# Optimization experiments

Measured on AMD Instinct MI355X. Metric: run time of the kernel, lower is better.

Reference implementation:

```python
import jax, jax.numpy as jnp
import numpy as np

B, M, N, R, FD = 128, 64, 64, 8, 128
BN_EPS = 1e-5
GS_EPS = 1e-8


def conv2d(x, w, b):
    # x: [B,C,H,W], w: [O,C,3,3] or [O,C,1,1]
    y = jax.lax.conv_general_dilated(x, w, (1, 1), 'SAME',
                                     dimension_numbers=('NCHW', 'OIHW', 'NCHW'))
    return y + b[None, :, None, None]


def complex_conv(x, wr, br, wi, bi):
    cr = conv2d(x, wr, br)
    ci = conv2d(x, wi, bi)
    return jnp.concatenate([cr - ci, cr + ci], axis=1)


def batchnorm(x, g, b):
    # training-mode BN over (B,H,W)
    mean = x.mean(axis=(0, 2, 3), keepdims=True)
    var = ((x - mean) ** 2).mean(axis=(0, 2, 3), keepdims=True)
    return g[None, :, None, None] * (x - mean) * jax.lax.rsqrt(var + BN_EPS) + b[None, :, None, None]


def gram_schmidt(mat):
    # mat: [B, M, R, 2]; sequential over R (hard data dependency), vectorized over batch
    Rr = mat.shape[2]
    basis = []  # list of (vr, vi), each [B, M]
    for j in range(Rr):
        vr, vi = mat[:, :, j, 0], mat[:, :, j, 1]
        for br_, bi_ in basis:
            dot_real = jnp.sum(vr * br_ + vi * bi_, axis=1, keepdims=True)
            denom = jnp.sum(br_ * br_ + bi_ * bi_, axis=1, keepdims=True) + GS_EPS
            coef = dot_real / denom  # only real part used (as in torch code)
            vr = vr - coef * br_
            vi = vi - coef * bi_
        nrm = jnp.sqrt(jnp.sum(vr * vr + vi * vi, axis=1, keepdims=True) + GS_EPS)
        basis.append((vr / nrm, vi / nrm))
    return jnp.stack([jnp.stack(p, axis=-1) for p in basis], axis=2)  # [B,M,R,2]


def setup_inputs() -> dict:
    key = jax.random.key(0)
    ks = jax.random.split(key, 32)
    def p(i, shape, fan_in):
        return jax.random.normal(ks[i], shape, jnp.float32) / np.sqrt(fan_in)
    inp = {
        'x':   jax.random.normal(ks[0], (B, M, N, 2), jnp.float32),
        'w1r': p(1, (32, 2, 3, 3), 2 * 9),   'b1r': jnp.zeros((32,), jnp.float32),
        'w1i': p(2, (32, 2, 3, 3), 2 * 9),   'b1i': jnp.zeros((32,), jnp.float32),
        'g1':  jnp.ones((64,), jnp.float32), 'be1': jnp.zeros((64,), jnp.float32),
        'w2r': p(3, (64, 64, 3, 3), 64 * 9), 'b2r': jnp.zeros((64,), jnp.float32),
        'w2i': p(4, (64, 64, 3, 3), 64 * 9), 'b2i': jnp.zeros((64,), jnp.float32),
        'g2':  jnp.ones((128,), jnp.float32), 'be2': jnp.zeros((128,), jnp.float32),
        'w3r': p(5, (FD, 128, 3, 3), 128 * 9), 'b3r': jnp.zeros((FD,), jnp.float32),
        'w3i': p(6, (FD, 128, 3, 3), 128 * 9), 'b3i': jnp.zeros((FD,), jnp.float32),
        'g3':  jnp.ones((2 * FD,), jnp.float32), 'be3': jnp.zeros((2 * FD,), jnp.float32),
        'wu':  p(7, (2 * R, 2 * FD), 2 * FD), 'bu': jnp.zeros((2 * R,), jnp.float32),
        'ws':  p(8, (R, 2 * FD), 2 * FD),     'bs': jnp.zeros((R,), jnp.float32),
        'wv':  p(9, (2 * R, 2 * FD), 2 * FD), 'bv': jnp.zeros((2 * R,), jnp.float32),
    }
    return inp


def forward(x, w1r, b1r, w1i, b1i, g1, be1, w2r, b2r, w2i, b2i, g2, be2,
            w3r, b3r, w3i, b3i, g3, be3, wu, bu, ws, bs, wv, bv):
    h = jnp.transpose(x, (0, 3, 1, 2))  # [B,2,M,N]
    h = jax.nn.relu(batchnorm(complex_conv(h, w1r, b1r, w1i, b1i), g1, be1))
    h = jax.nn.relu(batchnorm(complex_conv(h, w2r, b2r, w2i, b2i), g2, be2))
    h = jax.nn.relu(batchnorm(complex_conv(h, w3r, b3r, w3i, b3i), g3, be3))  # [B,2FD,M,N]
    # u branch: avg over W, 1x1 conv (= channel matmul), relu
    pu = h.mean(axis=3)                                      # [B,2FD,M]
    u = jax.nn.relu(jnp.einsum('bcm,oc->bom', pu, wu) + bu[None, :, None])  # [B,2R,M]
    u = jnp.transpose(u, (0, 2, 1)).reshape(-1, M, R, 2)     # channel c = 2j+part
    u = gram_schmidt(u)
    # s branch: global avg pool + linear + relu
    ps = h.mean(axis=(2, 3))                                 # [B,2FD]
    s = jax.nn.relu(ps @ ws.T + bs)                          # [B,R]
    # v branch: avg over H, 1x1 conv, relu
    pv = h.mean(axis=2)                                      # [B,2FD,N]
    v = jax.nn.relu(jnp.einsum('bcn,oc->bon', pv, wv) + bv[None, :, None])  # [B,2R,N]
    v = jnp.transpose(v, (0, 2, 1)).reshape(-1, N, R, 2)
    v = gram_schmidt(v)
    return (u, s, v)


def reference(x, w1r, b1r, w1i, b1i, g1, be1, w2r, b2r, w2i, b2i, g2, be2,
              w3r, b3r, w3i, b3i, g3, be3, wu, bu, ws, bs, wv, bv):
    return forward(x, w1r, b1r, w1i, b1i, g1, be1, w2r, b2r, w2i, b2i, g2, be2,
                   w3r, b3r, w3i, b3i, g3, be3, wu, bu, ws, bs, wv, bv)
```

## Files before the change

kernel.cpp:

```cpp
#include <hip/hip_runtime.h>

typedef _Float16 f16;
typedef __attribute__((ext_vector_type(8))) short short8;
typedef __attribute__((ext_vector_type(8))) _Float16 half8;
typedef __attribute__((ext_vector_type(4))) float f32x4;

#define DEV __device__ __forceinline__

DEV float h2f(short s) { f16 h; __builtin_memcpy(&h, &s, 2); return (float)h; }
DEV short f2h(float f) { f16 h = (f16)f; short s; __builtin_memcpy(&s, &h, 2); return s; }
DEV half8 s2h8(short8 s) { half8 h; __builtin_memcpy(&h, &s, 16); return h; }

DEV float wave_sum(float v) {
    #pragma unroll
    for (int m = 1; m < 64; m <<= 1) v += __shfl_xor(v, m);
    return v;
}

__global__ __launch_bounds__(256) void prep_w_k(
    const float* __restrict__ wr, const float* __restrict__ wi,
    f16* __restrict__ wf, int CIN, int COUT)
{
    int idx = blockIdx.x * 256 + threadIdx.x;
    int KC = CIN >> 5, NG = (2 * COUT) >> 4;
    int total = 9 * KC * NG * 512;
    if (idx >= total) return;
    int j = idx & 7, lane = (idx >> 3) & 63;
    int t9 = idx >> 9;
    int gg = t9 % NG, s = t9 / NG;
    int kc = s % KC, tap = s / KC;
    int n = gg * 16 + (lane & 15);
    int cin = kc * 32 + (lane >> 4) * 8 + j;
    int o = n < COUT ? n : n - COUT;
    float sgn = n < COUT ? -1.f : 1.f;
    float wv = wr[(o * CIN + cin) * 9 + tap] + sgn * wi[(o * CIN + cin) * 9 + tap];
    wf[idx] = (f16)wv;
}

__global__ __launch_bounds__(256) void conv1_k(
    const float* __restrict__ x,
    const float* __restrict__ w1r, const float* __restrict__ w1i,
    f16* __restrict__ out)
{
    int idx = blockIdx.x * 256 + threadIdx.x;
    int b = idx >> 12, p = idx & 4095;
    int m = p >> 6, n = p & 63;

    float v[2][9];
    #pragma unroll
    for (int dy = 0; dy < 3; ++dy)
        #pragma unroll
        for (int dx = 0; dx < 3; ++dx) {
            int yy = m + dy - 1, xx = n + dx - 1;
            bool ok = (yy >= 0 && yy < 64 && xx >= 0 && xx < 64);
            int base = ((b * 64 + (ok ? yy : 0)) * 64 + (ok ? xx : 0)) * 2;
            v[0][dy*3+dx] = ok ? x[base]     : 0.f;
            v[1][dy*3+dx] = ok ? x[base + 1] : 0.f;
        }

    float o1[64];
    #pragma unroll
    for (int o = 0; o < 32; ++o) {
        float cr = 0.f, ci = 0.f;
        #pragma unroll
        for (int c = 0; c < 2; ++c)
            #pragma unroll
            for (int k = 0; k < 9; ++k) {
                cr = fmaf(v[c][k], w1r[(o*2+c)*9 + k], cr);
                ci = fmaf(v[c][k], w1i[(o*2+c)*9 + k], ci);
            }
        o1[o]      = cr - ci;
        o1[32 + o] = cr + ci;
    }
    f16* ob = out + (size_t)idx * 64;
    #pragma unroll
    for (int grp = 0; grp < 8; ++grp) {
        short8 pk;
        #pragma unroll
        for (int k = 0; k < 8; ++k) pk[k] = f2h(o1[grp*8 + k]);
        *(short8*)(ob + grp * 8) = pk;
    }
}

template<int C8>
__global__ __launch_bounds__(256) void statsv_k(
    const f16* __restrict__ t, float* __restrict__ stats, int iters)
{
    const int C = C8 * 8;
    __shared__ float ls[2 * C];
    const int tid = threadIdx.x;
    const int cg = tid & (C8 - 1), pg = tid / C8;
    const int NG = 256 / C8;
    for (int u = tid; u < 2 * C; u += 256) ls[u] = 0.f;
    __syncthreads();
    float s8[8] = {0,0,0,0,0,0,0,0}, q8[8] = {0,0,0,0,0,0,0,0};
    size_t base = (size_t)blockIdx.x * NG * iters + pg;
    for (int i = 0; i < iters; ++i) {
        size_t pp = base + (size_t)i * NG;
        short8 r = *(const short8*)(t + pp * C + cg * 8);
        #pragma unroll
        for (int k = 0; k < 8; ++k) { float v = h2f(r[k]); s8[k] += v; q8[k] += v * v; }
    }
    #pragma unroll
    for (int k = 0; k < 8; ++k) {
        atomicAdd(&ls[cg*8 + k], s8[k]);
        atomicAdd(&ls[C + cg*8 + k], q8[k]);
    }
    __syncthreads();
    for (int u = tid; u < C; u += 256) {
        atomicAdd(&stats[u], ls[u]);
        atomicAdd(&stats[C + u], ls[C + u]);
    }
}

__global__ void bnparam_k(const float* __restrict__ stats,
                          const float* __restrict__ g, const float* __restrict__ be,
                          float* __restrict__ sc, int C)
{
    int c = threadIdx.x;
    if (c >= C) return;
    const float invN = 1.f / (128.f * 4096.f);
    float mean  = stats[c] * invN;
    float var   = stats[C + c] * invN - mean * mean;
    float scale = g[c] * rsqrtf(var + 1e-5f);
    sc[c]     = scale;
    sc[C + c] = be[c] - mean * scale;
}

template<int CIN, bool CHUNK>
__global__ __launch_bounds__(256, 4) void conv_mfma_k(
    const f16* __restrict__ in, const f16* __restrict__ wf,
    const float* __restrict__ scin, f16* __restrict__ outp,
    float* __restrict__ stats, int n0, int NG, int statsC, int ostride)
{
    constexpr int KQ = CIN / 32;
    constexpr int NSTEP = KQ * 9;
    __shared__ char actl[6*66*32*2];
    __shared__ char Bring[2][4096];
    __shared__ float lsts[4][64], lstq[4][64];
    const int flat = blockIdx.x;
    const int swzb = (flat & 7) * 256 + (flat >> 3);
    const int b = swzb >> 4, y0 = (swzb & 15) * 4;
    const int n0e = n0 + blockIdx.y * 64;
    const int tid = threadIdx.x, l = tid & 63, w = tid >> 6;
    const int li = l & 15, g = l >> 4;

    f32x4 acc[4][4];
    #pragma unroll
    for (int mf = 0; mf < 4; ++mf)
        #pragma unroll
        for (int nf = 0; nf < 4; ++nf)
            acc[mf][nf] = f32x4{0.f, 0.f, 0.f, 0.f};

    int swz[3];
    #pragma unroll
    for (int dx = 0; dx < 3; ++dx) swz[dx] = ((li + dx) & 7) << 4;

    const f16* wsrc0 = wf + ((size_t)((n0e >> 4) + w) << 9) + ((size_t)l << 3);
    auto issueB = [&](int st) {
        int kq = st / 9, tap = st - kq * 9;
        int s = tap * KQ + kq;
        const f16* src = wsrc0 + ((size_t)(s * NG) << 9);
        __builtin_amdgcn_global_load_lds(
            (const __attribute__((address_space(1))) void*)src,
            (__attribute__((address_space(3))) void*)&Bring[st & 1][w * 1024],
            16, 0, 0);
    };
    issueB(0);

    for (int st = 0; st < NSTEP; ++st) {
        const int kq = st / 9, tap = st - kq * 9;
        if (tap == 0) {
            half8 scl8, shf8;
            {
                int cb = kq*32 + (tid & 3) * 8;
                #pragma unroll
                for (int k = 0; k < 8; ++k) {
                    scl8[k] = (f16)scin[cb + k];
                    shf8[k] = (f16)scin[CIN + cb + k];
                }
            }
            #pragma unroll
            for (int i = 0; i < 7; ++i) {
                int u = tid + i * 256;
                if (u < 6*66*4) {
                    int r = u / 264, rem = u - r * 264;
                    int sx = rem >> 2, cg = rem & 3;
                    int srow = y0 - 1 + r, gx = sx - 1;
                    short8 pk = {0,0,0,0,0,0,0,0};
                    if (srow >= 0 && srow < 64 && gx >= 0 && gx < 64) {
                        short8 raw = *(const short8*)(in +
                            ((size_t)(b*4096 + srow*64 + gx)) * CIN + kq*32 + cg*8);
                        half8 rv = s2h8(raw) * scl8 + shf8;
                        short8 sr; __builtin_memcpy(&sr, &rv, 16);
                        pk = sr & ~(sr >> 15);
                    }
                    int off = ((r*66 + sx)*32 + cg*8)*2 ^ ((sx & 7) << 4);
                    *(short8*)(actl + off) = pk;
                }
            }
            __syncthreads();
        }
        if (st + 1 < NSTEP) issueB(st + 1);

        const char* Bl = Bring[st & 1];
        half8 bb[4];
        #pragma unroll
        for (int nf = 0; nf < 4; ++nf)
            bb[nf] = s2h8(*(const short8*)(Bl + nf*1024 + l*16));

        int dy = (tap * 11) >> 5, dx = tap - dy * 3;
        int r = w + dy;
        #pragma unroll
        for (int mf = 0; mf < 4; ++mf) {
            int sx = mf*16 + li + dx;
            half8 a = s2h8(*(const short8*)(actl + ((((r*66 + sx)*32) + g*8)*2 ^ swz[dx])));
            #pragma unroll
            for (int nf = 0; nf < 4; ++nf)
                acc[mf][nf] = __builtin_amdgcn_mfma_f32_16x16x32_f16(a, bb[nf], acc[mf][nf], 0, 0, 0);
        }
        __syncthreads();
    }

    #pragma unroll
    for (int nf = 0; nf < 4; ++nf) {
        float s = 0.f, q = 0.f;
        #pragma unroll
        for (int mf = 0; mf < 4; ++mf)
            #pragma unroll
            for (int reg = 0; reg < 4; ++reg) {
                float v = acc[mf][nf][reg];
                s += v; q += v * v;
            }
        s += __shfl_xor(s, 16); s += __shfl_xor(s, 32);
        q += __shfl_xor(q, 16); q += __shfl_xor(q, 32);
        if (l < 16) { lsts[w][nf*16 + l] = s; lstq[w][nf*16 + l] = q; }
    }
    __syncthreads();
    if (tid < 64) {
        const int sb = CHUNK ? 0 : n0e;
        float s = lsts[0][tid] + lsts[1][tid] + lsts[2][tid] + lsts[3][tid];
        float q = lstq[0][tid] + lstq[1][tid] + lstq[2][tid] + lstq[3][tid];
        atomicAdd(&stats[sb + tid], s);
        atomicAdd(&stats[statsC + sb + tid], q);
    }

    size_t rowbase = (size_t)b * 4096 + (size_t)(y0 + w) * 64;
    const int obase = CHUNK ? 0 : n0e;
    #pragma unroll
    for (int mf = 0; mf < 4; ++mf)
        #pragma unroll
        for (int nf = 0; nf < 4; ++nf) {
            int n = obase + nf*16 + li;
            #pragma unroll
            for (int reg = 0; reg < 4; ++reg) {
                int xx = mf*16 + g*4 + reg;
                outp[(rowbase + xx) * ostride + n] = (f16)acc[mf][nf][reg];
            }
        }
}

__global__ __launch_bounds__(256) void pool_k(
    const f16* __restrict__ t3c, const float* __restrict__ sc3c,
    float* __restrict__ pu, float* __restrict__ pv, int ncb)
{
    const int b = blockIdx.x, yh = blockIdx.y;
    const int t = threadIdx.x, cg = t & 7, xp = t >> 3;
    const int w = t >> 6, lane = t & 63;
    __shared__ float rq[4][16][64];
    float scl[8], shf[8];
    #pragma unroll
    for (int k = 0; k < 8; ++k) { scl[k] = sc3c[cg*8 + k]; shf[k] = sc3c[64 + cg*8 + k]; }
    float colacc[2][8];
    #pragma unroll
    for (int xi = 0; xi < 2; ++xi)
        #pragma unroll
        for (int k = 0; k < 8; ++k) colacc[xi][k] = 0.f;

    for (int yb = 0; yb < 2; ++yb) {
        for (int yy = 0; yy < 16; ++yy) {
            int y = yh*32 + yb*16 + yy;
            float rc[8];
            #pragma unroll
            for (int xi = 0; xi < 2; ++xi) {
                int xx = xp*2 + xi;
                short8 raw = *(const short8*)(t3c +
                    ((size_t)(b*4096 + y*64 + xx)) * 64 + cg*8);
                #pragma unroll
                for (int k = 0; k < 8; ++k) {
                    float v = fmaxf(fmaf(h2f(raw[k]), scl[k], shf[k]), 0.f);
                    colacc[xi][k] += v;
                    rc[k] = xi ? (rc[k] + v) : v;
                }
            }
            #pragma unroll
            for (int k = 0; k < 8; ++k) {
                rc[k] += __shfl_xor(rc[k], 8);
                rc[k] += __shfl_xor(rc[k], 16);
                rc[k] += __shfl_xor(rc[k], 32);
            }
            if (lane < 8) {
                #pragma unroll
                for (int k = 0; k < 8; ++k) rq[w][yy][lane*8 + k] = rc[k];
            }
        }
        __syncthreads();
        for (int u = t; u < 1024; u += 256) {
            int yy = u >> 6, c = u & 63;
            float v = rq[0][yy][c] + rq[1][yy][c] + rq[2][yy][c] + rq[3][yy][c];
            pu[((size_t)b*256 + ncb + c)*64 + (yh*32 + yb*16 + yy)] = v * (1.f/64.f);
        }
        __syncthreads();
    }
    #pragma unroll
    for (int xi = 0; xi < 2; ++xi)
        #pragma unroll
        for (int k = 0; k < 8; ++k)
            atomicAdd(&pv[((size_t)b*256 + ncb + cg*8 + k)*64 + xp*2 + xi],
                      colacc[xi][k] * (1.f/64.f));
}

__global__ __launch_bounds__(256) void headuv_k(
    const float* __restrict__ pool, const float* __restrict__ w,
    const float* __restrict__ bias, float* __restrict__ out)
{
    int b = blockIdx.x;
    int m = threadIdx.x & 63;
    int ob4 = threadIdx.x >> 6;
    float acc[4] = { bias[ob4], bias[ob4+4], bias[ob4+8], bias[ob4+12] };
    const float* pb = pool + (size_t)b * 256 * 64 + m;
    for (int c = 0; c < 256; ++c) {
        float v = pb[c * 64];
        #pragma unroll
        for (int i = 0; i < 4; ++i)
            acc[i] = fmaf(v, w[(ob4 + i*4) * 256 + c], acc[i]);
    }
    float* op = out + (size_t)b * 16 * 64 + m;
    #pragma unroll
    for (int i = 0; i < 4; ++i)
        op[(ob4 + i*4) * 64] = fmaxf(acc[i], 0.f);
}

__global__ __launch_bounds__(64) void heads_s_k(
    const float* __restrict__ pu, const float* __restrict__ wS,
    const float* __restrict__ bS, float* __restrict__ out)
{
    int b = blockIdx.x, lane = threadIdx.x;
    __shared__ float ls[256];
    for (int i = 0; i < 4; ++i) {
        const float* p = pu + ((size_t)b*256 + lane*4 + i) * 64;
        float s = 0.f;
        for (int m = 0; m < 64; ++m) s += p[m];
        ls[lane*4 + i] = s * (1.f/64.f);
    }
    __syncthreads();
    float acc[8] = {0,0,0,0,0,0,0,0};
    for (int c = lane; c < 256; c += 64) {
        float v = ls[c];
        #pragma unroll
        for (int o = 0; o < 8; ++o) acc[o] = fmaf(v, wS[o*256 + c], acc[o]);
    }
    #pragma unroll
    for (int o = 0; o < 8; ++o) acc[o] = wave_sum(acc[o]);
    if (lane == 0) {
        #pragma unroll
        for (int o = 0; o < 8; ++o)
            out[b*8 + o] = fmaxf(acc[o] + bS[o], 0.f);
    }
}

__global__ __launch_bounds__(64) void gs_k(
    const float* __restrict__ pre, float* __restrict__ out)
{
    int b = blockIdx.x, lane = threadIdx.x;
    const float* pb = pre + (size_t)b * 16 * 64 + lane;
    float vr[8], vi[8], den[8];
    #pragma unroll
    for (int j = 0; j < 8; ++j) { vr[j] = pb[(2*j)*64]; vi[j] = pb[(2*j+1)*64]; }

    #pragma unroll
    for (int j = 0; j < 8; ++j) {
        #pragma unroll
        for (int k = 0; k < j; ++k) {
            float d = wave_sum(vr[j]*vr[k] + vi[j]*vi[k]);
            float coef = d / den[k];
            vr[j] = fmaf(-coef, vr[k], vr[j]);
            vi[j] = fmaf(-coef, vi[k], vi[j]);
        }
        float n2 = wave_sum(vr[j]*vr[j] + vi[j]*vi[j]);
        float inv = 1.f / sqrtf(n2 + 1e-8f);
        vr[j] *= inv; vi[j] *= inv;
        float nn = wave_sum(vr[j]*vr[j] + vi[j]*vi[j]);
        den[j] = nn + 1e-8f;
    }
    float* ob = out + (size_t)b * 64 * 16 + lane * 16;
    #pragma unroll
    for (int j = 0; j < 8; ++j) { ob[j*2] = vr[j]; ob[j*2+1] = vi[j]; }
}

extern "C" void kernel_launch(void* const* d_in, const int* in_sizes, int n_in,
                              void* d_out, int out_size, void* d_ws, size_t ws_size,
                              hipStream_t stream)
{
    const float* x   = (const float*)d_in[0];
    const float* w1r = (const float*)d_in[1];
    const float* w1i = (const float*)d_in[3];
    const float* g1  = (const float*)d_in[5];
    const float* be1 = (const float*)d_in[6];
    const float* w2r = (const float*)d_in[7];
    const float* w2i = (const float*)d_in[9];
    const float* g2  = (const float*)d_in[11];
    const float* be2 = (const float*)d_in[12];
    const float* w3r = (const float*)d_in[13];
    const float* w3i = (const float*)d_in[15];
    const float* g3  = (const float*)d_in[17];
    const float* be3 = (const float*)d_in[18];
    const float* wu  = (const float*)d_in[19];
    const float* bu  = (const float*)d_in[20];
    const float* wS  = (const float*)d_in[21];
    const float* bS  = (const float*)d_in[22];
    const float* wv  = (const float*)d_in[23];
    const float* bv  = (const float*)d_in[24];
    float* out = (float*)d_out;

    char* ws = (char*)d_ws;
    f16*   t2     = (f16*)  (ws + 0);
    f16*   t1     = (f16*)  (ws + 134217728);
    f16*   t3c    = (f16*)  (ws + 134217728);
    float* upre   = (float*)(ws + 134217728);
    float* vpre   = (float*)(ws + 134742016);
    float* pu     = (float*)(ws + 201326592);
    float* pv     = (float*)(ws + 209715200);
    f16*   wfrag2 = (f16*)  (ws + 218103808);
    f16*   wfrag3 = (f16*)  (ws + 218103808);
    float* stats  = (float*)(ws + 219283456);
    float* scsh   = (float*)(ws + 219287040);
    float* stats1 = stats,  *stats2 = stats + 128;
    float* sc1    = scsh,   *sc2    = scsh  + 128, *sc3c = scsh + 384;

    hipMemsetAsync(stats, 0, 3584, stream);
    hipMemsetAsync(pv, 0, (size_t)128*256*64*4, stream);

    prep_w_k<<<288, 256, 0, stream>>>(w2r, w2i, wfrag2, 64, 64);

    conv1_k<<<2048, 256, 0, stream>>>(x, w1r, w1i, t1);
    statsv_k<8><<<1024, 256, 0, stream>>>(t1, stats1, 16);
    bnparam_k<<<1, 64, 0, stream>>>(stats1, g1, be1, sc1, 64);

    conv_mfma_k<64, false><<<dim3(2048, 2), 256, 0, stream>>>(
        t1, wfrag2, sc1, t2, stats2,
        0, 8, 128, 128);
    bnparam_k<<<1, 128, 0, stream>>>(stats2, g2, be2, sc2, 128);

    prep_w_k<<<1152, 256, 0, stream>>>(w3r, w3i, wfrag3, 128, 128);
    for (int nc = 0; nc < 4; ++nc) {
        conv_mfma_k<128, true><<<dim3(2048, 1), 256, 0, stream>>>(
            t2, wfrag3, sc2, t3c, stats + 384 + nc*128,
            nc*64, 16, 64, 64);
        bnparam_k<<<1, 64, 0, stream>>>(stats + 384 + nc*128, g3 + nc*64, be3 + nc*64, sc3c, 64);
        pool_k<<<dim3(128, 2), 256, 0, stream>>>(t3c, sc3c, pu, pv, nc*64);
    }

    headuv_k<<<128, 256, 0, stream>>>(pu, wu, bu, upre);
    headuv_k<<<128, 256, 0, stream>>>(pv, wv, bv, vpre);
    heads_s_k<<<128, 64, 0, stream>>>(pu, wS, bS, out + 131072);

    gs_k<<<128, 64, 0, stream>>>(upre, out);
    gs_k<<<128, 64, 0, stream>>>(vpre, out + 132096);
}
```

Baseline: 873.7 us.

## Group three conv K-steps per barrier with triple-buffered weight ring

Restructures the MFMA conv main loop so each iteration handles a group of three tap/K steps. The whole group's weight tiles are loaded into a three-slot LDS ring with one async global-to-LDS issue per group, and one barrier is paid per group instead of one per step. The larger weight ring roughly doubles LDS use per block, and launch bounds drop from 4 to 2 blocks per SM. This trades occupancy and latency hiding for fewer synchronisations.

```diff
diff --git a/kernel.cpp b/kernel.cpp
--- a/kernel.cpp
+++ b/kernel.cpp
@@ -128,15 +128,16 @@
 }
 
 template<int CIN, bool CHUNK>
-__global__ __launch_bounds__(256, 4) void conv_mfma_k(
+__global__ __launch_bounds__(256, 2) void conv_mfma_k(
     const f16* __restrict__ in, const f16* __restrict__ wf,
     const float* __restrict__ scin, f16* __restrict__ outp,
     float* __restrict__ stats, int n0, int NG, int statsC, int ostride)
 {
     constexpr int KQ = CIN / 32;
     constexpr int NSTEP = KQ * 9;
+    constexpr int G = NSTEP / 3;
     __shared__ char actl[6*66*32*2];
-    __shared__ char Bring[2][4096];
+    __shared__ char Bring[3][3][4096];
     __shared__ float lsts[4][64], lstq[4][64];
     const int flat = blockIdx.x;
     const int swzb = (flat & 7) * 256 + (flat >> 3);
@@ -157,20 +158,25 @@
     for (int dx = 0; dx < 3; ++dx) swz[dx] = ((li + dx) & 7) << 4;
 
     const f16* wsrc0 = wf + ((size_t)((n0e >> 4) + w) << 9) + ((size_t)l << 3);
-    auto issueB = [&](int st) {
-        int kq = st / 9, tap = st - kq * 9;
-        int s = tap * KQ + kq;
-        const f16* src = wsrc0 + ((size_t)(s * NG) << 9);
-        __builtin_amdgcn_global_load_lds(
-            (const __attribute__((address_space(1))) void*)src,
-            (__attribute__((address_space(3))) void*)&Bring[st & 1][w * 1024],
-            16, 0, 0);
+    auto issueB = [&](int gr) {
+        #pragma unroll
+        for (int j = 0; j < 3; ++j) {
+            int s = gr * 3 + j;
+            int kq = s / 9, tap = s - kq * 9;
+            int gs = tap * KQ + kq;
+            const f16* src = wsrc0 + ((size_t)(gs * NG) << 9);
+            __builtin_amdgcn_global_load_lds(
+                (const __attribute__((address_space(1))) void*)src,
+                (__attribute__((address_space(3))) void*)&Bring[gr % 3][j][w * 1024],
+                16, 0, 0);
+        }
     };
     issueB(0);
 
-    for (int st = 0; st < NSTEP; ++st) {
-        const int kq = st / 9, tap = st - kq * 9;
-        if (tap == 0) {
+    for (int gr = 0; gr < G; ++gr) {
+        if (gr % 3 == 0) {
+            const int kq = gr / 3;
+            __syncthreads();
             half8 scl8, shf8;
             {
                 int cb = kq*32 + (tid & 3) * 8;
@@ -199,27 +205,31 @@
                     *(short8*)(actl + off) = pk;
                 }
             }
-            __syncthreads();
-        }
-        if (st + 1 < NSTEP) issueB(st + 1);
-
-        const char* Bl = Bring[st & 1];
-        half8 bb[4];
-        #pragma unroll
-        for (int nf = 0; nf < 4; ++nf)
-            bb[nf] = s2h8(*(const short8*)(Bl + nf*1024 + l*16));
-
-        int dy = (tap * 11) >> 5, dx = tap - dy * 3;
-        int r = w + dy;
-        #pragma unroll
-        for (int mf = 0; mf < 4; ++mf) {
-            int sx = mf*16 + li + dx;
-            half8 a = s2h8(*(const short8*)(actl + ((((r*66 + sx)*32) + g*8)*2 ^ swz[dx])));
+        }
+        __syncthreads();
+        if (gr + 1 < G) issueB(gr + 1);
+
+        const char* Bl = &Bring[gr % 3][0][0];
+        #pragma unroll
+        for (int j = 0; j < 3; ++j) {
+            int s = gr * 3 + j;
+            int kq = s / 9, tap = s - kq * 9;
+            (void)kq;
+            half8 bb[4];
             #pragma unroll
             for (int nf = 0; nf < 4; ++nf)
-                acc[mf][nf] = __builtin_amdgcn_mfma_f32_16x16x32_f16(a, bb[nf], acc[mf][nf], 0, 0, 0);
-        }
-        __syncthreads();
+                bb[nf] = s2h8(*(const short8*)(Bl + (j*4 + nf)*1024 + l*16));
+            int dy = (tap * 11) >> 5, dx = tap - dy * 3;
+            int r = w + dy;
+            #pragma unroll
+            for (int mf = 0; mf < 4; ++mf) {
+                int sx = mf*16 + li + dx;
+                half8 a = s2h8(*(const short8*)(actl + ((((r*66 + sx)*32) + g*8)*2 ^ swz[dx])));
+                #pragma unroll
+                for (int nf = 0; nf < 4; ++nf)
+                    acc[mf][nf] = __builtin_amdgcn_mfma_f32_16x16x32_f16(a, bb[nf], acc[mf][nf], 0, 0, 0);
+            }
+        }
     }
 
     #pragma unroll
```

Result: no change. 877.6 us (+0.4%).
